# Optimization experiments

Hardware: AMD Instinct MI355X
Metric: run time of the kernel (lower is better)

Reference implementation:

```python
import jax, jax.numpy as jnp
import numpy as np
from jax import lax
import math

C = 512
B = 8
T = 8192


def _kaiser_sinc_filter1d(cutoff, half_width, kernel_size):
    # exact port of torch kaiser_sinc_filter1d (even kernel branch for k=12)
    half_size = kernel_size // 2
    delta_f = 4.0 * half_width
    A = 2.285 * (half_size - 1) * math.pi * delta_f + 7.95
    if A > 50.0:
        beta = 0.1102 * (A - 8.7)
    elif A >= 21.0:
        beta = 0.5842 * (A - 21.0) ** 0.4 + 0.07886 * (A - 21.0)
    else:
        beta = 0.0
    window = np.kaiser(kernel_size, beta)  # symmetric == torch periodic=False
    if kernel_size % 2 == 0:
        time = np.arange(-half_size, half_size) + 0.5
    else:
        time = np.arange(kernel_size) - half_size
    filt = 2.0 * cutoff * window * np.sinc(2.0 * cutoff * time)
    filt = filt / filt.sum()
    return filt.astype(np.float32)  # [kernel_size]


def _make_up_down_filters(channels, ratio=2, kernel_size=12):
    f = _kaiser_sinc_filter1d(0.5 / ratio, 0.5 / ratio, kernel_size)
    # upsample weight: polyphase split of f*ratio -> [2,1,6], repeat per channel -> [2C,1,6]
    w = f * ratio
    p0, p1 = w[0::2], w[1::2]
    up = np.stack([p0, p1], axis=0)[:, None, :]            # [2,1,6]
    up = np.tile(up, (channels, 1, 1))                     # [2C,1,6]
    # downsample (low-pass) weight: [C,1,12]
    down = np.tile(f.reshape(1, 1, kernel_size), (channels, 1, 1))
    return jnp.asarray(up), jnp.asarray(down)


def _conv1d(x, w, stride=1, padding=0, dilation=1, groups=1):
    return lax.conv_general_dilated(
        x, w, window_strides=(stride,), padding=[(padding, padding)],
        rhs_dilation=(dilation,), dimension_numbers=('NCH', 'OIH', 'NCH'),
        feature_group_count=groups)


def _snake_beta(x, alpha, beta):
    # alpha_logscale=True
    a = jnp.exp(alpha)[None, :, None]
    b = jnp.exp(beta)[None, :, None]
    return x + (1.0 - jnp.cos(2.0 * a * x)) / (2.0 * b + 1e-9)


def _upsample(x, up_filt):
    b, c, _ = x.shape
    xp = jnp.pad(x, ((0, 0), (0, 0), (2, 3)))
    out = _conv1d(xp, up_filt, groups=c)                   # [B, 2C, T']
    out = out.reshape(b, c, 2, -1)                         # (channel, phase) split
    out = jnp.transpose(out, (0, 1, 3, 2)).reshape(b, c, -1)  # interleave phases
    return out[..., 2:-2]                                  # [B, C, 2T-4]


def _downsample(x, down_filt):
    c = x.shape[1]
    return _conv1d(x, down_filt, stride=2, padding=5, groups=c)


def _activation1d(x, alpha, beta, up_filt, down_filt):
    x = _upsample(x, up_filt)
    x = _snake_beta(x, alpha, beta)
    return _downsample(x, down_filt)


def _wn_weight(v, g):
    # weight_norm (dim=0): w = g * v / ||v||, norm over (in, k) per output channel
    norm = jnp.sqrt(jnp.sum(v * v, axis=(1, 2), keepdims=True))
    return g[:, None, None] * v / norm


def setup_inputs() -> dict:
    key = jax.random.key(0)
    ks = jax.random.split(key, 12)
    x = jax.random.normal(ks[0], (B, C, T), dtype=jnp.float32)
    alpha1 = 0.1 * jax.random.normal(ks[1], (C,), dtype=jnp.float32)
    beta1 = 0.1 * jax.random.normal(ks[2], (C,), dtype=jnp.float32)
    alpha2 = 0.1 * jax.random.normal(ks[3], (C,), dtype=jnp.float32)
    beta2 = 0.1 * jax.random.normal(ks[4], (C,), dtype=jnp.float32)
    scale = 1.0 / np.sqrt(C * 3)
    v1 = scale * jax.random.normal(ks[5], (C, C, 3), dtype=jnp.float32)
    g1 = jax.random.uniform(ks[6], (C,), dtype=jnp.float32, minval=0.5, maxval=1.5)
    b1 = 0.01 * jax.random.normal(ks[7], (C,), dtype=jnp.float32)
    v2 = scale * jax.random.normal(ks[8], (C, C, 3), dtype=jnp.float32)
    g2 = jax.random.uniform(ks[9], (C,), dtype=jnp.float32, minval=0.5, maxval=1.5)
    b2 = 0.01 * jax.random.normal(ks[10], (C,), dtype=jnp.float32)
    up_filt, down_filt = _make_up_down_filters(C)
    return dict(x=x, alpha1=alpha1, beta1=beta1, alpha2=alpha2, beta2=beta2,
                v1=v1, g1=g1, b1=b1, v2=v2, g2=g2, b2=b2,
                up_filt=up_filt, down_filt=down_filt)


def reference(x, alpha1, beta1, alpha2, beta2, v1, g1, b1, v2, g2, b2,
              up_filt, down_filt):
    w1 = _wn_weight(v1, g1)
    w2 = _wn_weight(v2, g2)
    # dilation = (1,3,5) -> convs1 uses dilation[0] = 1, padding = get_padding(3,1) = 1
    xt = _activation1d(x, alpha1, beta1, up_filt, down_filt)    # [B,C,T-2]
    xt = _conv1d(xt, w1, padding=1, dilation=1) + b1[None, :, None]
    xt = _activation1d(xt, alpha2, beta2, up_filt, down_filt)   # [B,C,T-4]
    xt = _conv1d(xt, w2, padding=1, dilation=1) + b2[None, :, None]
    x_residual = x[..., :xt.shape[2]]                            # narrow(2, 0, T-4)
    return xt + x_residual
```

## Files before the change

### kernel.cpp

```cpp
#include <hip/hip_runtime.h>
#include <hip/hip_bf16.h>

#define CCH 512
#define BATCH 8
#define TLEN 8192
#define RPITCH ((size_t)TLEN * CCH)

using f32x4 = __attribute__((ext_vector_type(4))) float;
using s16x8 = __attribute__((ext_vector_type(8))) short;
using s16x4 = __attribute__((ext_vector_type(4))) short;
using s16x2 = __attribute__((ext_vector_type(2))) short;

__device__ __forceinline__ float b2f(short s) {
    union { unsigned int i; float f; } u; u.i = ((unsigned int)(unsigned short)s) << 16; return u.f;
}
__device__ __forceinline__ short f2b(float f) {
    __hip_bfloat16 h = __float2bfloat16(f);
    return *reinterpret_cast<short*>(&h);
}

__device__ __forceinline__ void glds16(const void* g, void* l) {
    __builtin_amdgcn_global_load_lds(
        (const __attribute__((address_space(1))) unsigned int*)g,
        (__attribute__((address_space(3))) unsigned int*)l, 16, 0, 0);
}

__global__ __launch_bounds__(256) void wn_pack_kernel(const float* __restrict__ v,
                                                      const float* __restrict__ g,
                                                      short* __restrict__ wp)
{
    int co = blockIdx.x;
    const float* vr = v + (size_t)co * (CCH * 3);
    float s = 0.f;
    for (int i = threadIdx.x; i < CCH * 3; i += 256) { float xv = vr[i]; s += xv * xv; }
#pragma unroll
    for (int off = 32; off > 0; off >>= 1) s += __shfl_down(s, off);
    __shared__ float red[4];
    int lane = threadIdx.x & 63, wv = threadIdx.x >> 6;
    if (lane == 0) red[wv] = s;
    __syncthreads();
    float tot = red[0] + red[1] + red[2] + red[3];
    float scale = g[co] / sqrtf(tot);
    int row = co & 127;
    int swz = ((row >> 1) & 3) << 3;
    for (int i = threadIdx.x; i < CCH * 3; i += 256) {
        int ci = i / 3, tap = i - ci * 3;
        size_t dst = ((size_t)(((ci >> 5) * 4 + (co >> 7)) * 3 + tap)) * 4096
                     + (size_t)row * 32 + ((ci & 31) ^ swz);
        wp[dst] = f2b(vr[i] * scale);
    }
}

__global__ __launch_bounds__(256) void transpose_kernel2(const float* __restrict__ x,
                                                         short* __restrict__ out)
{
    __shared__ float ls[64][65];
    int tid = threadIdx.x;
    int t0 = blockIdx.x * 64, c0 = blockIdx.y * 64, b = blockIdx.z;
    const float* xb = x + (size_t)b * CCH * TLEN;
#pragma unroll
    for (int p = 0; p < 4; ++p) {
        int c = p * 16 + (tid >> 4);
        int t4 = (tid & 15) * 4;
        f32x4 v = *(const f32x4*)&xb[(size_t)(c0 + c) * TLEN + t0 + t4];
#pragma unroll
        for (int i = 0; i < 4; ++i) ls[c][t4 + i] = v[i];
    }
    __syncthreads();
    short* ob = out + (size_t)b * RPITCH;
#pragma unroll
    for (int p = 0; p < 4; ++p) {
        int t = p * 16 + (tid >> 4);
        int c4 = (tid & 15) * 4;
        s16x4 o;
#pragma unroll
        for (int i = 0; i < 4; ++i) o[i] = f2b(ls[c4 + i][t]);
        *(s16x4*)(ob + (size_t)(t0 + t) * CCH + c0 + c4) = o;
    }
}

#define ALT 128
__global__ __launch_bounds__(256) void act_kernel(
    const short* __restrict__ in, short* __restrict__ out,
    const float* __restrict__ alpha, const float* __restrict__ beta,
    const float* __restrict__ upf, const float* __restrict__ dwf,
    int Tin, int Tout)
{
    int tid = threadIdx.x;
    int c2 = tid * 2;
    int b = blockIdx.z;
    int t0 = blockIdx.x * ALT;
    const short* ib = in + (size_t)b * RPITCH + c2;
    short* ob = out + (size_t)b * RPITCH + c2;

    float ph0[6], ph1[6], fw[12];
#pragma unroll
    for (int m = 0; m < 6; ++m) { ph0[m] = upf[m]; ph1[m] = upf[6 + m]; }
#pragma unroll
    for (int k = 0; k < 12; ++k) fw[k] = dwf[k];

    float twoa[2], inv2b[2];
#pragma unroll
    for (int ch = 0; ch < 2; ++ch) {
        twoa[ch]  = 2.f * __expf(alpha[c2 + ch]);
        inv2b[ch] = 1.f / (2.f * __expf(beta[c2 + ch]) + 1e-9f);
    }
    int Ls = 2 * Tin - 4;

    auto ldx2 = [&](int t, float* dst) {
        if (t >= 0 && t < Tin) {
            s16x2 v = *(const s16x2*)(ib + (size_t)t * CCH);
            dst[0] = b2f(v[0]); dst[1] = b2f(v[1]);
        } else { dst[0] = 0.f; dst[1] = 0.f; }
    };

    float xa[12][2];
#pragma unroll
    for (int i = 0; i < 12; ++i) ldx2(t0 - 4 + i, xa[i]);
    float sr[12][2];
#pragma unroll
    for (int i = 0; i < 12; ++i) {
        int j = 2 * t0 - 5 + i;
        int xoff = ((i - 3) >> 1) + 2;
        const float* ph = ((i + 1) & 1) ? ph1 : ph0;
        bool ok = (j >= 0 && j < Ls);
#pragma unroll
        for (int ch = 0; ch < 2; ++ch) {
            float u = 0.f;
#pragma unroll
            for (int m = 0; m < 6; ++m) u += ph[m] * xa[xoff + m][ch];
            sr[i][ch] = ok ? (u + (1.f - __cosf(twoa[ch] * u)) * inv2b[ch]) : 0.f;
        }
    }
    float xw[7][2];
#pragma unroll
    for (int m = 0; m < 6; ++m) { xw[m][0] = xa[6 + m][0]; xw[m][1] = xa[6 + m][1]; }
    ldx2(t0 + 8, xw[6]);

#pragma unroll 4
    for (int it = 0; it < ALT; ++it) {
        int t = t0 + it;
        float y[2] = {0.f, 0.f};
#pragma unroll
        for (int k = 0; k < 12; ++k) {
            y[0] += fw[k] * sr[k][0];
            y[1] += fw[k] * sr[k][1];
        }
        if (t < Tout) {
            s16x2 o; o[0] = f2b(y[0]); o[1] = f2b(y[1]);
            *(s16x2*)(ob + (size_t)t * CCH) = o;
        }
        bool ok1 = (2 * t + 7 < Ls), ok2 = (2 * t + 8 < Ls);
        float s1[2], s2[2];
#pragma unroll
        for (int ch = 0; ch < 2; ++ch) {
            float u1 = 0.f, u2 = 0.f;
#pragma unroll
            for (int m = 0; m < 6; ++m) {
                u1 += ph1[m] * xw[m][ch];
                u2 += ph0[m] * xw[m + 1][ch];
            }
            s1[ch] = ok1 ? (u1 + (1.f - __cosf(twoa[ch] * u1)) * inv2b[ch]) : 0.f;
            s2[ch] = ok2 ? (u2 + (1.f - __cosf(twoa[ch] * u2)) * inv2b[ch]) : 0.f;
        }
#pragma unroll
        for (int i = 0; i < 10; ++i) { sr[i][0] = sr[i + 2][0]; sr[i][1] = sr[i + 2][1]; }
        sr[10][0] = s1[0]; sr[10][1] = s1[1];
        sr[11][0] = s2[0]; sr[11][1] = s2[1];
#pragma unroll
        for (int m = 0; m < 6; ++m) { xw[m][0] = xw[m + 1][0]; xw[m][1] = xw[m + 1][1]; }
        ldx2(t + 9, xw[6]);
    }
}

template <int MODE>
__global__ __launch_bounds__(256) void conv_mfma(
    const short* __restrict__ xin, const short* __restrict__ wp,
    const float* __restrict__ bias, const float* __restrict__ resid,
    float* __restrict__ outF, short* __restrict__ outT, int rows)
{
    constexpr int WB = 3 * 128 * 32;
    constexpr int IB = 132 * 32;
    __shared__ __align__(16) short lds[2 * (WB + IB)];

    int tid = threadIdx.x;
    int wave = tid >> 6, lane = tid & 63;
    int quad = lane >> 4, l16 = lane & 15;
    int wm = wave >> 1, wn = wave & 1;
    int bx = blockIdx.x;
    int cog = bx & 3, tt = bx >> 2;
    int t0 = tt * 128, b = blockIdx.z;

    const short* inb = xin + (size_t)b * RPITCH;
    bool interior = (t0 >= 1) && (t0 + 129 <= rows);

    auto stage = [&](int cc, int pb) {
        short* base = lds + pb * (WB + IB);
        short* wl = base;
        short* il = base + WB;
        const short* wsrc = wp + (size_t)(cc * 4 + cog) * WB;
#pragma unroll
        for (int p = 0; p < 6; ++p) {
            int seg = wave * 6 + p;
            glds16(wsrc + seg * 512 + lane * 8, wl + seg * 512);
        }
        const short* isrc = inb + (size_t)(t0 - 1) * CCH + cc * 32;
        if (interior) {
#pragma unroll
            for (int p = 0; p < 2; ++p) {
                int seg0 = (p * 4 + wave) * 64;
                int s = seg0 + lane;
                int u = s ^ ((s >> 3) & 3);
                glds16(isrc + (size_t)(u >> 2) * CCH + (u & 3) * 8, il + seg0 * 8);
            }
            if (wave == 0 && lane < 8) {
                int s = 512 + lane;
                glds16(isrc + (size_t)(s >> 2) * CCH + (s & 3) * 8, il + 512 * 8);
            }
        } else {
            for (int s = tid; s < 520; s += 256) {
                int gt = t0 - 1 + (s >> 2);
                s16x8 v = 0;
                if (gt >= 0 && gt < rows)
                    v = *(const s16x8*)(inb + (size_t)gt * CCH + cc * 32 + (s & 3) * 8);
                int ps = s ^ ((s >> 3) & 3);
                *(s16x8*)(il + ps * 8) = v;
            }
        }
    };

    f32x4 acc[4][4];
#pragma unroll
    for (int i = 0; i < 4; ++i)
#pragma unroll
        for (int j = 0; j < 4; ++j) acc[i][j] = 0.f;

    stage(0, 0);
    __syncthreads();

    for (int cc = 0; cc < 16; ++cc) {
        int pb = cc & 1;
        if (cc < 15) stage(cc + 1, pb ^ 1);
        const short* base = lds + pb * (WB + IB);
        const short* wl = base;
        const short* il = base + WB;
#pragma unroll
        for (int tap = 0; tap < 3; ++tap) {
            s16x8 af[4], bv[4];
#pragma unroll
            for (int mf = 0; mf < 4; ++mf) {
                int row = wm * 64 + mf * 16 + l16;
                int off = (quad * 8) ^ (((row >> 1) & 3) << 3);
                af[mf] = *(const s16x8*)(wl + tap * 4096 + row * 32 + off);
            }
#pragma unroll
            for (int nf = 0; nf < 4; ++nf) {
                int row = wn * 64 + nf * 16 + l16 + tap;
                int off = (quad * 8) ^ (((row >> 1) & 3) << 3);
                bv[nf] = *(const s16x8*)(il + row * 32 + off);
            }
#pragma unroll
            for (int mf = 0; mf < 4; ++mf)
#pragma unroll
                for (int nf = 0; nf < 4; ++nf)
                    acc[mf][nf] = __builtin_amdgcn_mfma_f32_16x16x32_bf16(
                        af[mf], bv[nf], acc[mf][nf], 0, 0, 0);
        }
        __syncthreads();
    }

    f32x4 b4[4];
#pragma unroll
    for (int mf = 0; mf < 4; ++mf)
        b4[mf] = *(const f32x4*)(bias + cog * 128 + wm * 64 + mf * 16 + quad * 4);

    if (MODE == 0) {
        short* ot = lds;
#pragma unroll
        for (int mf = 0; mf < 4; ++mf)
#pragma unroll
            for (int nf = 0; nf < 4; ++nf) {
                int t = wn * 64 + nf * 16 + l16;
                int co = wm * 64 + mf * 16 + quad * 4;
                s16x4 o;
#pragma unroll
                for (int r = 0; r < 4; ++r) o[r] = f2b(acc[mf][nf][r] + b4[mf][r]);
                *(s16x4*)(ot + t * 136 + co) = o;
            }
        __syncthreads();
#pragma unroll
        for (int rr = 0; rr < 8; ++rr) {
            int idx = rr * 256 + tid;
            int tr = idx >> 4, c8 = (idx & 15) * 8;
            int t = t0 + tr;
            if (t < rows)
                *(s16x8*)(outT + (size_t)b * RPITCH + (size_t)t * CCH + cog * 128 + c8)
                    = *(const s16x8*)(ot + tr * 136 + c8);
        }
    } else {
        float* of = (float*)lds;
#pragma unroll
        for (int h = 0; h < 2; ++h) {
            if (wm == h) {
#pragma unroll
                for (int mf = 0; mf < 4; ++mf)
#pragma unroll
                    for (int nf = 0; nf < 4; ++nf) {
                        int t = wn * 64 + nf * 16 + l16;
#pragma unroll
                        for (int r = 0; r < 4; ++r)
                            of[(mf * 16 + quad * 4 + r) * 132 + t] = acc[mf][nf][r] + b4[mf][r];
                    }
            }
            __syncthreads();
#pragma unroll
            for (int rr = 0; rr < 8; ++rr) {
                int idx = rr * 256 + tid;
                int row = idx >> 5, c4 = (idx & 31) * 4;
                int co = cog * 128 + h * 64 + row;
                int t = t0 + c4;
                f32x4 v = *(const f32x4*)(of + row * 132 + c4);
                size_t ro = (size_t)b * CCH + co;
                const float* rrow = resid + ro * TLEN;
                float* orow = outF + ro * (size_t)rows;
                if (t + 3 < rows) {
                    f32x4 rv = *(const f32x4*)(rrow + t);
                    f32x4 ov;
#pragma unroll
                    for (int i = 0; i < 4; ++i) ov[i] = v[i] + rv[i];
                    *(f32x4*)(orow + t) = ov;
                } else {
#pragma unroll
                    for (int i = 0; i < 4; ++i)
                        if (t + i < rows) orow[t + i] = v[i] + rrow[t + i];
                }
            }
            __syncthreads();
        }
    }
}

extern "C" void kernel_launch(void* const* d_in, const int* in_sizes, int n_in,
                              void* d_out, int out_size, void* d_ws, size_t ws_size,
                              hipStream_t stream)
{
    const float* x      = (const float*)d_in[0];
    const float* alpha1 = (const float*)d_in[1];
    const float* beta1  = (const float*)d_in[2];
    const float* alpha2 = (const float*)d_in[3];
    const float* beta2  = (const float*)d_in[4];
    const float* v1     = (const float*)d_in[5];
    const float* g1     = (const float*)d_in[6];
    const float* b1     = (const float*)d_in[7];
    const float* v2     = (const float*)d_in[8];
    const float* g2     = (const float*)d_in[9];
    const float* b2     = (const float*)d_in[10];
    const float* upf    = (const float*)d_in[11];
    const float* dwf    = (const float*)d_in[12];
    float* out = (float*)d_out;

    const int T1 = TLEN - 2;
    const int T2 = TLEN - 4;

    char* wsb = (char*)d_ws;
    short* w1p = (short*)wsb;
    short* w2p = w1p + (size_t)CCH * CCH * 3;
    short* bufX = w2p + (size_t)CCH * CCH * 3;
    short* bufY = bufX + (size_t)BATCH * RPITCH;

    wn_pack_kernel<<<CCH, 256, 0, stream>>>(v1, g1, w1p);
    wn_pack_kernel<<<CCH, 256, 0, stream>>>(v2, g2, w2p);

    transpose_kernel2<<<dim3(TLEN / 64, CCH / 64, BATCH), 256, 0, stream>>>(x, bufX);

    act_kernel<<<dim3((TLEN + ALT - 1) / ALT, 1, BATCH), 256, 0, stream>>>(
        bufX, bufY, alpha1, beta1, upf, dwf, TLEN, T1);

    conv_mfma<0><<<dim3(256, 1, BATCH), 256, 0, stream>>>(
        bufY, w1p, b1, nullptr, nullptr, bufX, T1);

    act_kernel<<<dim3((T1 + ALT - 1) / ALT, 1, BATCH), 256, 0, stream>>>(
        bufX, bufY, alpha2, beta2, upf, dwf, T1, T2);

    conv_mfma<1><<<dim3(256, 1, BATCH), 256, 0, stream>>>(
        bufY, w2p, b2, x, out, nullptr, T2);
}
```

Baseline: 676.9 us.

## Load conv weights directly into registers and retune activation kernel tiling

The conv kernel stops staging weight tiles through shared memory. Each wave now loads its weight fragments straight from global memory into two register buffers, prefetching one channel chunk ahead, while shared memory holds only the double-buffered input tile. The weight-pack kernel drops its XOR swizzle to match the new direct-load layout. The activation kernel halves its time tile for more blocks, adds an occupancy hint, and prefetches input rows further ahead. This cuts shared-memory traffic and footprint in the conv, at the cost of much higher register pressure and weight reads served from L2.

```diff
diff --git a/kernel.cpp b/kernel.cpp
--- a/kernel.cpp
+++ b/kernel.cpp
@@ -41,12 +41,10 @@
     __syncthreads();
     float tot = red[0] + red[1] + red[2] + red[3];
     float scale = g[co] / sqrtf(tot);
-    int row = co & 127;
-    int swz = ((row >> 1) & 3) << 3;
     for (int i = threadIdx.x; i < CCH * 3; i += 256) {
         int ci = i / 3, tap = i - ci * 3;
         size_t dst = ((size_t)(((ci >> 5) * 4 + (co >> 7)) * 3 + tap)) * 4096
-                     + (size_t)row * 32 + ((ci & 31) ^ swz);
+                     + (size_t)(co & 127) * 32 + (ci & 31);
         wp[dst] = f2b(vr[i] * scale);
     }
 }
@@ -79,8 +77,8 @@
     }
 }
 
-#define ALT 128
-__global__ __launch_bounds__(256) void act_kernel(
+#define ALT 64
+__global__ __launch_bounds__(256, 4) void act_kernel(
     const short* __restrict__ in, short* __restrict__ out,
     const float* __restrict__ alpha, const float* __restrict__ beta,
     const float* __restrict__ upf, const float* __restrict__ dwf,
@@ -132,10 +130,12 @@
             sr[i][ch] = ok ? (u + (1.f - __cosf(twoa[ch] * u)) * inv2b[ch]) : 0.f;
         }
     }
-    float xw[7][2];
+    float xw[9][2];
 #pragma unroll
     for (int m = 0; m < 6; ++m) { xw[m][0] = xa[6 + m][0]; xw[m][1] = xa[6 + m][1]; }
-    ldx2(t0 + 8, xw[6]);
+    ldx2(t0 + 8,  xw[6]);
+    ldx2(t0 + 9,  xw[7]);
+    ldx2(t0 + 10, xw[8]);
 
 #pragma unroll 4
     for (int it = 0; it < ALT; ++it) {
@@ -168,20 +168,19 @@
         sr[10][0] = s1[0]; sr[10][1] = s1[1];
         sr[11][0] = s2[0]; sr[11][1] = s2[1];
 #pragma unroll
-        for (int m = 0; m < 6; ++m) { xw[m][0] = xw[m + 1][0]; xw[m][1] = xw[m + 1][1]; }
-        ldx2(t + 9, xw[6]);
+        for (int m = 0; m < 8; ++m) { xw[m][0] = xw[m + 1][0]; xw[m][1] = xw[m + 1][1]; }
+        ldx2(t + 11, xw[8]);
     }
 }
 
 template <int MODE>
-__global__ __launch_bounds__(256) void conv_mfma(
+__global__ __launch_bounds__(256, 2) void conv_mfma(
     const short* __restrict__ xin, const short* __restrict__ wp,
     const float* __restrict__ bias, const float* __restrict__ resid,
     float* __restrict__ outF, short* __restrict__ outT, int rows)
 {
-    constexpr int WB = 3 * 128 * 32;
     constexpr int IB = 132 * 32;
-    __shared__ __align__(16) short lds[2 * (WB + IB)];
+    __shared__ __align__(16) short lds[17408];
 
     int tid = threadIdx.x;
     int wave = tid >> 6, lane = tid & 63;
@@ -194,16 +193,8 @@
     const short* inb = xin + (size_t)b * RPITCH;
     bool interior = (t0 >= 1) && (t0 + 129 <= rows);
 
-    auto stage = [&](int cc, int pb) {
-        short* base = lds + pb * (WB + IB);
-        short* wl = base;
-        short* il = base + WB;
-        const short* wsrc = wp + (size_t)(cc * 4 + cog) * WB;
-#pragma unroll
-        for (int p = 0; p < 6; ++p) {
-            int seg = wave * 6 + p;
-            glds16(wsrc + seg * 512 + lane * 8, wl + seg * 512);
-        }
+    auto stage = [&](int cc, int pbuf) {
+        short* il = lds + pbuf * IB;
         const short* isrc = inb + (size_t)(t0 - 1) * CCH + cc * 32;
         if (interior) {
 #pragma unroll
@@ -229,30 +220,26 @@
         }
     };
 
+    const short* wbase = wp + (size_t)(wm * 64 + l16) * 32 + quad * 8;
+    auto loadA = [&](int cc, s16x8 (&ar)[3][4]) {
+        const short* wc = wbase + (size_t)((cc * 4 + cog) * 3) * 4096;
+#pragma unroll
+        for (int tap = 0; tap < 3; ++tap)
+#pragma unroll
+            for (int mf = 0; mf < 4; ++mf)
+                ar[tap][mf] = *(const s16x8*)(wc + tap * 4096 + mf * 512);
+    };
+
     f32x4 acc[4][4];
 #pragma unroll
     for (int i = 0; i < 4; ++i)
 #pragma unroll
         for (int j = 0; j < 4; ++j) acc[i][j] = 0.f;
 
-    stage(0, 0);
-    __syncthreads();
-
-    for (int cc = 0; cc < 16; ++cc) {
-        int pb = cc & 1;
-        if (cc < 15) stage(cc + 1, pb ^ 1);
-        const short* base = lds + pb * (WB + IB);
-        const short* wl = base;
-        const short* il = base + WB;
+    auto compute = [&](const s16x8 (&ar)[3][4], const short* il) {
 #pragma unroll
         for (int tap = 0; tap < 3; ++tap) {
-            s16x8 af[4], bv[4];
-#pragma unroll
-            for (int mf = 0; mf < 4; ++mf) {
-                int row = wm * 64 + mf * 16 + l16;
-                int off = (quad * 8) ^ (((row >> 1) & 3) << 3);
-                af[mf] = *(const s16x8*)(wl + tap * 4096 + row * 32 + off);
-            }
+            s16x8 bv[4];
 #pragma unroll
             for (int nf = 0; nf < 4; ++nf) {
                 int row = wn * 64 + nf * 16 + l16 + tap;
@@ -264,8 +251,25 @@
 #pragma unroll
                 for (int nf = 0; nf < 4; ++nf)
                     acc[mf][nf] = __builtin_amdgcn_mfma_f32_16x16x32_bf16(
-                        af[mf], bv[nf], acc[mf][nf], 0, 0, 0);
-        }
+                        ar[tap][mf], bv[nf], acc[mf][nf], 0, 0, 0);
+        }
+    };
+
+    s16x8 a0[3][4], a1[3][4];
+    loadA(0, a0);
+    loadA(1, a1);
+    stage(0, 0);
+    __syncthreads();
+
+    for (int cc2 = 0; cc2 < 8; ++cc2) {
+        int ccA = 2 * cc2;
+        stage(ccA + 1, 1);
+        compute(a0, lds);
+        if (ccA + 2 < 16) loadA(ccA + 2, a0);
+        __syncthreads();
+        if (ccA + 2 < 16) stage(ccA + 2, 0);
+        compute(a1, lds + IB);
+        if (ccA + 3 < 16) loadA(ccA + 3, a1);
         __syncthreads();
     }
 
```

Measured after the change: 700.2 us. 3.4% more time.

## Enlarge conv tile to 256 timesteps and deepen act-kernel prefetch window

Applied to the files above, without the earlier changes.

The conv MFMA kernel now gives each block 256 time steps instead of 128, so each wave holds twice as many accumulators. Each weight fragment read from LDS is reused across more MFMAs, and the grid halves. The compute phase is also wrapped in s_setprio. The activation kernel shrinks its time tile to 64, sets a 4-blocks-per-CU launch bound and prefetches input rows two steps further ahead. The costs are higher register pressure and LDS use per conv block, and fewer blocks (1024) to spread across the GPU.

```diff
diff --git a/kernel.cpp b/kernel.cpp
--- a/kernel.cpp
+++ b/kernel.cpp
@@ -79,8 +79,8 @@
     }
 }
 
-#define ALT 128
-__global__ __launch_bounds__(256) void act_kernel(
+#define ALT 64
+__global__ __launch_bounds__(256, 4) void act_kernel(
     const short* __restrict__ in, short* __restrict__ out,
     const float* __restrict__ alpha, const float* __restrict__ beta,
     const float* __restrict__ upf, const float* __restrict__ dwf,
@@ -132,10 +132,12 @@
             sr[i][ch] = ok ? (u + (1.f - __cosf(twoa[ch] * u)) * inv2b[ch]) : 0.f;
         }
     }
-    float xw[7][2];
+    float xw[9][2];
 #pragma unroll
     for (int m = 0; m < 6; ++m) { xw[m][0] = xa[6 + m][0]; xw[m][1] = xa[6 + m][1]; }
-    ldx2(t0 + 8, xw[6]);
+    ldx2(t0 + 8,  xw[6]);
+    ldx2(t0 + 9,  xw[7]);
+    ldx2(t0 + 10, xw[8]);
 
 #pragma unroll 4
     for (int it = 0; it < ALT; ++it) {
@@ -168,20 +170,21 @@
         sr[10][0] = s1[0]; sr[10][1] = s1[1];
         sr[11][0] = s2[0]; sr[11][1] = s2[1];
 #pragma unroll
-        for (int m = 0; m < 6; ++m) { xw[m][0] = xw[m + 1][0]; xw[m][1] = xw[m + 1][1]; }
-        ldx2(t + 9, xw[6]);
+        for (int m = 0; m < 8; ++m) { xw[m][0] = xw[m + 1][0]; xw[m][1] = xw[m + 1][1]; }
+        ldx2(t + 11, xw[8]);
     }
 }
 
 template <int MODE>
-__global__ __launch_bounds__(256) void conv_mfma(
+__global__ __launch_bounds__(256, 1) void conv_mfma(
     const short* __restrict__ xin, const short* __restrict__ wp,
     const float* __restrict__ bias, const float* __restrict__ resid,
     float* __restrict__ outF, short* __restrict__ outT, int rows)
 {
     constexpr int WB = 3 * 128 * 32;
-    constexpr int IB = 132 * 32;
-    __shared__ __align__(16) short lds[2 * (WB + IB)];
+    constexpr int IB = 260 * 32;
+    constexpr int PB = WB + IB;
+    __shared__ __align__(16) short lds[2 * PB];
 
     int tid = threadIdx.x;
     int wave = tid >> 6, lane = tid & 63;
@@ -189,13 +192,13 @@
     int wm = wave >> 1, wn = wave & 1;
     int bx = blockIdx.x;
     int cog = bx & 3, tt = bx >> 2;
-    int t0 = tt * 128, b = blockIdx.z;
+    int t0 = tt * 256, b = blockIdx.z;
 
     const short* inb = xin + (size_t)b * RPITCH;
-    bool interior = (t0 >= 1) && (t0 + 129 <= rows);
+    bool interior = (t0 >= 1) && (t0 + 259 <= rows);
 
     auto stage = [&](int cc, int pb) {
-        short* base = lds + pb * (WB + IB);
+        short* base = lds + pb * PB;
         short* wl = base;
         short* il = base + WB;
         const short* wsrc = wp + (size_t)(cc * 4 + cog) * WB;
@@ -207,18 +210,19 @@
         const short* isrc = inb + (size_t)(t0 - 1) * CCH + cc * 32;
         if (interior) {
 #pragma unroll
-            for (int p = 0; p < 2; ++p) {
-                int seg0 = (p * 4 + wave) * 64;
-                int s = seg0 + lane;
+            for (int p = 0; p < 4; ++p) {
+                int sg = wave * 4 + p;
+                int s = sg * 64 + lane;
                 int u = s ^ ((s >> 3) & 3);
-                glds16(isrc + (size_t)(u >> 2) * CCH + (u & 3) * 8, il + seg0 * 8);
-            }
-            if (wave == 0 && lane < 8) {
-                int s = 512 + lane;
-                glds16(isrc + (size_t)(s >> 2) * CCH + (s & 3) * 8, il + 512 * 8);
+                glds16(isrc + (size_t)(u >> 2) * CCH + (u & 3) * 8, il + sg * 512);
+            }
+            if (wave == 0 && lane < 16) {
+                int s = 1024 + lane;
+                int u = s ^ ((s >> 3) & 3);
+                glds16(isrc + (size_t)(u >> 2) * CCH + (u & 3) * 8, il + 1024 * 8);
             }
         } else {
-            for (int s = tid; s < 520; s += 256) {
+            for (int s = tid; s < 1040; s += 256) {
                 int gt = t0 - 1 + (s >> 2);
                 s16x8 v = 0;
                 if (gt >= 0 && gt < rows)
@@ -229,24 +233,20 @@
         }
     };
 
-    f32x4 acc[4][4];
+    f32x4 acc[4][8];
 #pragma unroll
     for (int i = 0; i < 4; ++i)
 #pragma unroll
-        for (int j = 0; j < 4; ++j) acc[i][j] = 0.f;
-
-    stage(0, 0);
-    __syncthreads();
-
-    for (int cc = 0; cc < 16; ++cc) {
-        int pb = cc & 1;
-        if (cc < 15) stage(cc + 1, pb ^ 1);
-        const short* base = lds + pb * (WB + IB);
+        for (int j = 0; j < 8; ++j) acc[i][j] = 0.f;
+
+    auto compute = [&](int pb) {
+        const short* base = lds + pb * PB;
         const short* wl = base;
         const short* il = base + WB;
+        __builtin_amdgcn_s_setprio(1);
 #pragma unroll
         for (int tap = 0; tap < 3; ++tap) {
-            s16x8 af[4], bv[4];
+            s16x8 af[4], bv[8];
 #pragma unroll
             for (int mf = 0; mf < 4; ++mf) {
                 int row = wm * 64 + mf * 16 + l16;
@@ -254,18 +254,27 @@
                 af[mf] = *(const s16x8*)(wl + tap * 4096 + row * 32 + off);
             }
 #pragma unroll
-            for (int nf = 0; nf < 4; ++nf) {
-                int row = wn * 64 + nf * 16 + l16 + tap;
+            for (int nf = 0; nf < 8; ++nf) {
+                int row = wn * 128 + nf * 16 + l16 + tap;
                 int off = (quad * 8) ^ (((row >> 1) & 3) << 3);
                 bv[nf] = *(const s16x8*)(il + row * 32 + off);
             }
 #pragma unroll
             for (int mf = 0; mf < 4; ++mf)
 #pragma unroll
-                for (int nf = 0; nf < 4; ++nf)
+                for (int nf = 0; nf < 8; ++nf)
                     acc[mf][nf] = __builtin_amdgcn_mfma_f32_16x16x32_bf16(
                         af[mf], bv[nf], acc[mf][nf], 0, 0, 0);
         }
+        __builtin_amdgcn_s_setprio(0);
+    };
+
+    stage(0, 0);
+    __syncthreads();
+
+    for (int cc = 0; cc < 16; ++cc) {
+        if (cc < 15) stage(cc + 1, (cc + 1) & 1);
+        compute(cc & 1);
         __syncthreads();
     }
 
@@ -279,8 +288,8 @@
 #pragma unroll
         for (int mf = 0; mf < 4; ++mf)
 #pragma unroll
-            for (int nf = 0; nf < 4; ++nf) {
-                int t = wn * 64 + nf * 16 + l16;
+            for (int nf = 0; nf < 8; ++nf) {
+                int t = wn * 128 + nf * 16 + l16;
                 int co = wm * 64 + mf * 16 + quad * 4;
                 s16x4 o;
 #pragma unroll
@@ -289,7 +298,7 @@
             }
         __syncthreads();
 #pragma unroll
-        for (int rr = 0; rr < 8; ++rr) {
+        for (int rr = 0; rr < 16; ++rr) {
             int idx = rr * 256 + tid;
             int tr = idx >> 4, c8 = (idx & 15) * 8;
             int t = t0 + tr;
@@ -305,21 +314,21 @@
 #pragma unroll
                 for (int mf = 0; mf < 4; ++mf)
 #pragma unroll
-                    for (int nf = 0; nf < 4; ++nf) {
-                        int t = wn * 64 + nf * 16 + l16;
+                    for (int nf = 0; nf < 8; ++nf) {
+                        int t = wn * 128 + nf * 16 + l16;
 #pragma unroll
                         for (int r = 0; r < 4; ++r)
-                            of[(mf * 16 + quad * 4 + r) * 132 + t] = acc[mf][nf][r] + b4[mf][r];
+                            of[(mf * 16 + quad * 4 + r) * 260 + t] = acc[mf][nf][r] + b4[mf][r];
                     }
             }
             __syncthreads();
 #pragma unroll
-            for (int rr = 0; rr < 8; ++rr) {
+            for (int rr = 0; rr < 16; ++rr) {
                 int idx = rr * 256 + tid;
-                int row = idx >> 5, c4 = (idx & 31) * 4;
+                int row = idx >> 6, c4 = (idx & 63) * 4;
                 int co = cog * 128 + h * 64 + row;
                 int t = t0 + c4;
-                f32x4 v = *(const f32x4*)(of + row * 132 + c4);
+                f32x4 v = *(const f32x4*)(of + row * 260 + c4);
                 size_t ro = (size_t)b * CCH + co;
                 const float* rrow = resid + ro * TLEN;
                 float* orow = outF + ro * (size_t)rows;
@@ -376,12 +385,12 @@
     act_kernel<<<dim3((TLEN + ALT - 1) / ALT, 1, BATCH), 256, 0, stream>>>(
         bufX, bufY, alpha1, beta1, upf, dwf, TLEN, T1);
 
-    conv_mfma<0><<<dim3(256, 1, BATCH), 256, 0, stream>>>(
+    conv_mfma<0><<<dim3(4 * 32, 1, BATCH), 256, 0, stream>>>(
         bufY, w1p, b1, nullptr, nullptr, bufX, T1);
 
     act_kernel<<<dim3((T1 + ALT - 1) / ALT, 1, BATCH), 256, 0, stream>>>(
         bufX, bufY, alpha2, beta2, upf, dwf, T1, T2);
 
-    conv_mfma<1><<<dim3(256, 1, BATCH), 256, 0, stream>>>(
+    conv_mfma<1><<<dim3(4 * 32, 1, BATCH), 256, 0, stream>>>(
         bufY, w2p, b2, x, out, nullptr, T2);
 }
```

Result: slower. 731.4 us (+8.0%).
